# Optimization experiments

Hardware: AMD Instinct MI355X
Metric: run time of the kernel (lower is better)

## Reference

```python
import jax, jax.numpy as jnp
import numpy as np

B, S, HID = 2, 2048, 2048
H, HKV, DH = 32, 8, 64
GROUPS = H // HKV
SCALE = DH ** -0.5
ROPE_THETA = 10000.0
NEG_INF = jnp.finfo(jnp.float32).min


def setup_inputs() -> dict:
    key = jax.random.key(0)
    ks = jax.random.split(key, 6)
    hidden_states = jax.random.normal(ks[0], (B, S, HID), dtype=jnp.float32)
    # true rotary embeddings (HF Llama style): inv_freq over half dim, duplicated
    inv_freq = 1.0 / (ROPE_THETA ** (np.arange(0, DH, 2, dtype=np.float32) / DH))
    freqs = np.arange(S, dtype=np.float32)[:, None] * inv_freq[None, :]  # [S, DH/2]
    emb = np.concatenate([freqs, freqs], axis=-1)                        # [S, DH]
    cos = jnp.broadcast_to(jnp.asarray(np.cos(emb), jnp.float32), (B, S, DH))
    sin = jnp.broadcast_to(jnp.asarray(np.sin(emb), jnp.float32), (B, S, DH))
    # additive causal mask [1,1,S,S]
    causal = jnp.tril(jnp.ones((S, S), dtype=bool))
    attention_mask = jnp.where(causal, 0.0, NEG_INF)[None, None].astype(jnp.float32)
    std = 0.02
    Wq = jax.random.normal(ks[1], (H * DH, HID), dtype=jnp.float32) * std
    Wk = jax.random.normal(ks[2], (HKV * DH, HID), dtype=jnp.float32) * std
    Wv = jax.random.normal(ks[3], (HKV * DH, HID), dtype=jnp.float32) * std
    Wo = jax.random.normal(ks[4], (HID, H * DH), dtype=jnp.float32) * std
    return {"hidden_states": hidden_states, "cos": cos, "sin": sin,
            "attention_mask": attention_mask, "Wq": Wq, "Wk": Wk, "Wv": Wv, "Wo": Wo}


def _rotate_half(x):
    x1, x2 = jnp.split(x, 2, axis=-1)
    return jnp.concatenate([-x2, x1], axis=-1)


def reference(hidden_states, cos, sin, attention_mask, Wq, Wk, Wv, Wo):
    b, s, _ = hidden_states.shape
    # projections -> [B, H(kv), S, DH]
    q = (hidden_states @ Wq.T).reshape(b, s, H, DH).transpose(0, 2, 1, 3)
    k = (hidden_states @ Wk.T).reshape(b, s, HKV, DH).transpose(0, 2, 1, 3)
    v = (hidden_states @ Wv.T).reshape(b, s, HKV, DH).transpose(0, 2, 1, 3)
    # RoPE (cos/sin: [B,S,DH] -> broadcast over head axis)
    c = cos[:, None, :, :]
    sn = sin[:, None, :, :]
    q = q * c + _rotate_half(q) * sn
    k = k * c + _rotate_half(k) * sn
    # GQA: repeat kv heads
    k = jnp.repeat(k, GROUPS, axis=1)  # [B,H,S,DH]
    v = jnp.repeat(v, GROUPS, axis=1)
    # eager attention: full [B,H,S,S] scores in memory
    scores = jnp.einsum('bhqd,bhkd->bhqk', q, k) * SCALE + attention_mask[:, :, :, :s]
    attn = jax.nn.softmax(scores, axis=-1)
    out = jnp.einsum('bhqk,bhkd->bhqd', attn, v)
    out = out.transpose(0, 2, 1, 3).reshape(b, s, H * DH)
    return out @ Wo.T
```

## Files before the change

### kernel.cpp

```cpp
#include <hip/hip_runtime.h>
#include <hip/hip_bf16.h>
#include <cstdint>
#include <cstddef>

#define B_    2
#define S_    2048
#define HID_  2048
#define H_    32
#define HKV_  8
#define DH_   64
#define SC2_  0.1803368801111244f

typedef __bf16 bf16;
typedef bf16  bf16x2 __attribute__((ext_vector_type(2)));
typedef bf16  bf16x4 __attribute__((ext_vector_type(4)));
typedef bf16  bf16x8 __attribute__((ext_vector_type(8)));
typedef float f32x4  __attribute__((ext_vector_type(4)));
typedef float f32x16 __attribute__((ext_vector_type(16)));
typedef uint32_t u32x2 __attribute__((ext_vector_type(2)));

typedef __attribute__((address_space(3))) uint32_t  lds_u32_t;
typedef __attribute__((address_space(1))) const uint32_t glob_u32_t;

__device__ __forceinline__ void async16(const void* g, void* l) {
    __builtin_amdgcn_global_load_lds((glob_u32_t*)g, (lds_u32_t*)l, 16, 0, 0);
}

__device__ __forceinline__ bf16x8 cvt8(float4 a, float4 b) {
    bf16x8 r;
    r[0] = (bf16)a.x; r[1] = (bf16)a.y; r[2] = (bf16)a.z; r[3] = (bf16)a.w;
    r[4] = (bf16)b.x; r[5] = (bf16)b.y; r[6] = (bf16)b.z; r[7] = (bf16)b.w;
    return r;
}

__device__ __forceinline__ uint32_t pkbf(float a, float b) {
    bf16x2 t; t[0] = (bf16)a; t[1] = (bf16)b;
    return __builtin_bit_cast(uint32_t, t);
}
__device__ __forceinline__ bf16x8 mk8(uint32_t a, uint32_t b, uint32_t c, uint32_t d) {
    union { uint32_t u[4]; bf16x8 v; } t;
    t.u[0] = a; t.u[1] = b; t.u[2] = c; t.u[3] = d;
    return t.v;
}

#define WAIT_N_BARRIER(N_ASM)                              \
    asm volatile(N_ASM ::: "memory");                      \
    __builtin_amdgcn_s_barrier();                          \
    __builtin_amdgcn_sched_barrier(0);

#define END_BARRIER()                                      \
    __builtin_amdgcn_sched_barrier(0);                     \
    __builtin_amdgcn_s_barrier();

__global__ __launch_bounds__(256) void cvt_all_kernel(
    const float* __restrict__ X,  const float* __restrict__ Wq,
    const float* __restrict__ Wk, const float* __restrict__ Wv,
    const float* __restrict__ Wo,
    bf16* __restrict__ Xb,  bf16* __restrict__ Wqb, bf16* __restrict__ Wkb,
    bf16* __restrict__ Wvb, bf16* __restrict__ Wob)
{
    const int i = blockIdx.x * 256 + threadIdx.x;
    const float* src; bf16* dst; int off;
    if (i < 1048576)      { src = X;  dst = Xb;  off = i; }
    else if (i < 1572864) { src = Wq; dst = Wqb; off = i - 1048576; }
    else if (i < 1703936) { src = Wk; dst = Wkb; off = i - 1572864; }
    else if (i < 1835008) { src = Wv; dst = Wvb; off = i - 1703936; }
    else                  { src = Wo; dst = Wob; off = i - 1835008; }
    float4 a = ((const float4*)src)[2 * off];
    float4 b = ((const float4*)src)[2 * off + 1];
    ((bf16x8*)dst)[off] = cvt8(a, b);
}

__global__ __launch_bounds__(256) void gemm_qkv_kernel(
    const bf16* __restrict__ A,
    const bf16* __restrict__ Wqb, const bf16* __restrict__ Wkb,
    const bf16* __restrict__ Wvb,
    const float* __restrict__ cs, const float* __restrict__ sn,
    bf16* __restrict__ Qo, bf16* __restrict__ Ko, bf16* __restrict__ Vt)
{
    __shared__ bf16 a_lds[2][128 * 64];
    __shared__ bf16 b_lds[2][128 * 64];

    const int tid  = threadIdx.x;
    const int wave = tid >> 6;
    const int lane = tid & 63;
    const int quad = lane >> 4;
    const int l16  = lane & 15;
    const int wm   = wave >> 1;
    const int wn   = wave & 1;

    const int idx = blockIdx.x + 32 * blockIdx.y;
    const int swz = (idx & 7) * 96 + (idx >> 3);
    const int m0  = (swz & 31) * 128;
    const int n0  = (swz >> 5) * 128;

    f32x4 acc[4][4];
    #pragma unroll
    for (int mt = 0; mt < 4; ++mt)
        #pragma unroll
        for (int nt = 0; nt < 4; ++nt)
            acc[mt][nt] = (f32x4){0.f, 0.f, 0.f, 0.f};

    int srow[4], sgcol[4];
    const bf16* browp[4];
    #pragma unroll
    for (int i = 0; i < 4; ++i) {
        const int e = tid * 8 + i * 2048;
        srow[i] = e >> 6;
        const int chunk = (e >> 3) & 7;
        sgcol[i] = (chunk ^ (srow[i] & 7)) << 3;
        const int n = n0 + srow[i];
        browp[i] = (n < 2048) ? (Wqb + (size_t)n * HID_)
                 : (n < 2560) ? (Wkb + (size_t)(n - 2048) * HID_)
                              : (Wvb + (size_t)(n - 2560) * HID_);
    }

    #pragma unroll
    for (int i = 0; i < 4; ++i) {
        async16(A + (size_t)(m0 + srow[i]) * HID_ + sgcol[i],
                &a_lds[0][tid * 8 + i * 2048]);
        async16(browp[i] + sgcol[i],
                &b_lds[0][tid * 8 + i * 2048]);
    }

    for (int k0 = 0; k0 < HID_; k0 += 64) {
        const int cur = (k0 >> 6) & 1;
        if (k0 + 64 < HID_) {
            #pragma unroll
            for (int i = 0; i < 4; ++i) {
                async16(A + (size_t)(m0 + srow[i]) * HID_ + k0 + 64 + sgcol[i],
                        &a_lds[cur ^ 1][tid * 8 + i * 2048]);
                async16(browp[i] + k0 + 64 + sgcol[i],
                        &b_lds[cur ^ 1][tid * 8 + i * 2048]);
            }
            WAIT_N_BARRIER("s_waitcnt vmcnt(8)");
        } else {
            WAIT_N_BARRIER("s_waitcnt vmcnt(0)");
        }
        const bf16* al = a_lds[cur];
        const bf16* bl = b_lds[cur];
        #pragma unroll
        for (int ks = 0; ks < 2; ++ks) {
            bf16x8 af[4], bfr[4];
            #pragma unroll
            for (int mt = 0; mt < 4; ++mt) {
                const int row = wm * 64 + mt * 16 + l16;
                const int c = (ks * 4 + quad) ^ (row & 7);
                af[mt] = *(const bf16x8*)(&al[row * 64 + c * 8]);
            }
            #pragma unroll
            for (int nt = 0; nt < 4; ++nt) {
                const int row = wn * 64 + nt * 16 + l16;
                const int c = (ks * 4 + quad) ^ (row & 7);
                bfr[nt] = *(const bf16x8*)(&bl[row * 64 + c * 8]);
            }
            #pragma unroll
            for (int mt = 0; mt < 4; ++mt)
                #pragma unroll
                for (int nt = 0; nt < 4; ++nt)
                    acc[mt][nt] = __builtin_amdgcn_mfma_f32_16x16x32_bf16(
                        af[mt], bfr[nt], acc[mt][nt], 0, 0, 0);
        }
        END_BARRIER();
    }

    const int nw = n0 + wn * 64;
    const int d  = l16;
    #pragma unroll
    for (int mt = 0; mt < 4; ++mt) {
        #pragma unroll
        for (int r = 0; r < 4; ++r) {
            const int m  = m0 + wm * 64 + mt * 16 + quad * 4 + r;
            const int bb = m >> 11;
            const int ss = m & (S_ - 1);
            const float v0 = acc[mt][0][r], v1 = acc[mt][1][r];
            const float v2 = acc[mt][2][r], v3 = acc[mt][3][r];
            if (nw < 2048) {
                const int h = nw >> 6;
                bf16* dp = Qo + ((size_t)(bb * H_ + h) * S_ + ss) * DH_;
                const float* cp = cs + ((size_t)bb * S_ + ss) * DH_;
                const float* sp = sn + ((size_t)bb * S_ + ss) * DH_;
                dp[ 0 + d] = (bf16)((v0 * cp[ 0 + d] - v2 * sp[ 0 + d]) * SC2_);
                dp[16 + d] = (bf16)((v1 * cp[16 + d] - v3 * sp[16 + d]) * SC2_);
                dp[32 + d] = (bf16)((v2 * cp[32 + d] + v0 * sp[32 + d]) * SC2_);
                dp[48 + d] = (bf16)((v3 * cp[48 + d] + v1 * sp[48 + d]) * SC2_);
            } else if (nw < 2560) {
                const int h = (nw - 2048) >> 6;
                bf16* dp = Ko + ((size_t)(bb * HKV_ + h) * S_ + ss) * DH_;
                const float* cp = cs + ((size_t)bb * S_ + ss) * DH_;
                const float* sp = sn + ((size_t)bb * S_ + ss) * DH_;
                dp[ 0 + d] = (bf16)(v0 * cp[ 0 + d] - v2 * sp[ 0 + d]);
                dp[16 + d] = (bf16)(v1 * cp[16 + d] - v3 * sp[16 + d]);
                dp[32 + d] = (bf16)(v2 * cp[32 + d] + v0 * sp[32 + d]);
                dp[48 + d] = (bf16)(v3 * cp[48 + d] + v1 * sp[48 + d]);
            } else {
                const int h = (nw - 2560) >> 6;
                bf16* dp = Vt + ((size_t)(bb * HKV_ + h) * DH_) * S_ + ss;
                dp[(size_t)( 0 + d) * S_] = (bf16)v0;
                dp[(size_t)(16 + d) * S_] = (bf16)v1;
                dp[(size_t)(32 + d) * S_] = (bf16)v2;
                dp[(size_t)(48 + d) * S_] = (bf16)v3;
            }
        }
    }
}

__global__ __launch_bounds__(256) void gemm_out_kernel(
    const bf16* __restrict__ A, const bf16* __restrict__ Wb,
    float* __restrict__ Y)
{
    __shared__ bf16 a_lds[2][128 * 64];
    __shared__ bf16 b_lds[2][128 * 64];

    const int tid  = threadIdx.x;
    const int wave = tid >> 6;
    const int lane = tid & 63;
    const int quad = lane >> 4;
    const int l16  = lane & 15;
    const int wm   = wave >> 1;
    const int wn   = wave & 1;

    const int idx = blockIdx.x + 32 * blockIdx.y;
    const int swz = (idx & 7) * 64 + (idx >> 3);
    const int m0  = (swz & 31) * 128;
    const int n0  = (swz >> 5) * 128;

    f32x4 acc[4][4];
    #pragma unroll
    for (int mt = 0; mt < 4; ++mt)
        #pragma unroll
        for (int nt = 0; nt < 4; ++nt)
            acc[mt][nt] = (f32x4){0.f, 0.f, 0.f, 0.f};

    int srow[4], sgcol[4];
    #pragma unroll
    for (int i = 0; i < 4; ++i) {
        const int e = tid * 8 + i * 2048;
        srow[i] = e >> 6;
        const int chunk = (e >> 3) & 7;
        sgcol[i] = (chunk ^ (srow[i] & 7)) << 3;
    }

    #pragma unroll
    for (int i = 0; i < 4; ++i) {
        async16(A + (size_t)(m0 + srow[i]) * HID_ + sgcol[i],
                &a_lds[0][tid * 8 + i * 2048]);
        async16(Wb + (size_t)(n0 + srow[i]) * HID_ + sgcol[i],
                &b_lds[0][tid * 8 + i * 2048]);
    }

    for (int k0 = 0; k0 < HID_; k0 += 64) {
        const int cur = (k0 >> 6) & 1;
        if (k0 + 64 < HID_) {
            #pragma unroll
            for (int i = 0; i < 4; ++i) {
                async16(A + (size_t)(m0 + srow[i]) * HID_ + k0 + 64 + sgcol[i],
                        &a_lds[cur ^ 1][tid * 8 + i * 2048]);
                async16(Wb + (size_t)(n0 + srow[i]) * HID_ + k0 + 64 + sgcol[i],
                        &b_lds[cur ^ 1][tid * 8 + i * 2048]);
            }
            WAIT_N_BARRIER("s_waitcnt vmcnt(8)");
        } else {
            WAIT_N_BARRIER("s_waitcnt vmcnt(0)");
        }
        const bf16* al = a_lds[cur];
        const bf16* bl = b_lds[cur];
        #pragma unroll
        for (int ks = 0; ks < 2; ++ks) {
            bf16x8 af[4], bfr[4];
            #pragma unroll
            for (int mt = 0; mt < 4; ++mt) {
                const int row = wm * 64 + mt * 16 + l16;
                const int c = (ks * 4 + quad) ^ (row & 7);
                af[mt] = *(const bf16x8*)(&al[row * 64 + c * 8]);
            }
            #pragma unroll
            for (int nt = 0; nt < 4; ++nt) {
                const int row = wn * 64 + nt * 16 + l16;
                const int c = (ks * 4 + quad) ^ (row & 7);
                bfr[nt] = *(const bf16x8*)(&bl[row * 64 + c * 8]);
            }
            #pragma unroll
            for (int mt = 0; mt < 4; ++mt)
                #pragma unroll
                for (int nt = 0; nt < 4; ++nt)
                    acc[mt][nt] = __builtin_amdgcn_mfma_f32_16x16x32_bf16(
                        af[mt], bfr[nt], acc[mt][nt], 0, 0, 0);
        }
        END_BARRIER();
    }

    #pragma unroll
    for (int mt = 0; mt < 4; ++mt)
        #pragma unroll
        for (int nt = 0; nt < 4; ++nt)
            #pragma unroll
            for (int r = 0; r < 4; ++r) {
                const int m = m0 + wm * 64 + mt * 16 + quad * 4 + r;
                const int n = n0 + wn * 64 + nt * 16 + l16;
                Y[(size_t)m * HID_ + n] = acc[mt][nt][r];
            }
}

__global__ __launch_bounds__(256) void attn_kernel(
    const bf16* __restrict__ Q, const bf16* __restrict__ K,
    const bf16* __restrict__ Vt, bf16* __restrict__ O)
{
    __shared__ bf16 k_lds[2][64 * 64];
    __shared__ bf16 v_lds[2][64 * 64];

    const int tid  = threadIdx.x;
    const int wave = tid >> 6;
    const int lane = tid & 63;
    const int l32  = lane & 31;
    const int half = lane >> 5;
    const int h  = blockIdx.y;
    const int b  = blockIdx.z;
    const int hkv = h >> 2;

    const bf16* Qg = Q  + (size_t)(b * H_ + h) * S_ * DH_;
    const bf16* Kg = K  + (size_t)(b * HKV_ + hkv) * S_ * DH_;
    const bf16* Vg = Vt + ((size_t)(b * HKV_ + hkv) * DH_) * S_;

    const int srow0  = tid >> 3;
    const int scolsw = ((tid & 7) ^ ((tid >> 3) & 7)) << 3;

    #pragma unroll 1
    for (int ph = 0; ph < 2; ++ph) {
        const int qt  = ph == 0 ? (int)blockIdx.x : (15 - (int)blockIdx.x);
        const int q0  = qt * 128;
        const int qb0 = q0 + wave * 32;
        const int qa  = qb0 + l32;

        bf16x8 qf[4];
        #pragma unroll
        for (int c = 0; c < 4; ++c)
            qf[c] = *(const bf16x8*)(Qg + (size_t)qa * DH_ + c * 16 + half * 8);

        f32x16 o_acc[2];
        #pragma unroll
        for (int dt = 0; dt < 2; ++dt)
            #pragma unroll
            for (int e = 0; e < 16; ++e) o_acc[dt][e] = 0.f;
        float m_i = -1e30f, l_i = 0.f;

        const int nkt = 2 * qt + 2;

        #pragma unroll
        for (int i = 0; i < 2; ++i) {
            const int row = srow0 + i * 32;
            async16(Kg + (size_t)row * DH_ + scolsw, &k_lds[0][tid * 8 + i * 2048]);
            async16(Vg + (size_t)row * S_  + scolsw, &v_lds[0][tid * 8 + i * 2048]);
        }

        for (int kt = 0; kt < nkt; ++kt) {
            if (kt + 1 < nkt) {
                bf16* kb = k_lds[(kt + 1) & 1];
                bf16* vb = v_lds[(kt + 1) & 1];
                #pragma unroll
                for (int i = 0; i < 2; ++i) {
                    const int row = srow0 + i * 32;
                    async16(Kg + (size_t)((kt + 1) * 64 + row) * DH_ + scolsw,
                            kb + tid * 8 + i * 2048);
                    async16(Vg + (size_t)row * S_ + (kt + 1) * 64 + scolsw,
                            vb + tid * 8 + i * 2048);
                }
                WAIT_N_BARRIER("s_waitcnt vmcnt(4)");
            } else {
                WAIT_N_BARRIER("s_waitcnt vmcnt(0)");
            }

            if (kt * 64 <= qb0 + 31) {
                const bf16* kb = k_lds[kt & 1];
                const bf16* vb = v_lds[kt & 1];
                const bool act1 = (kt * 64 + 32) <= (qb0 + 31);

                f32x16 s0, s1;
                {
                    bf16x8 kf[4];
                    #pragma unroll
                    for (int c = 0; c < 4; ++c) {
                        const int col = ((2 * c + half) ^ (l32 & 7)) << 3;
                        kf[c] = *(const bf16x8*)(kb + l32 * 64 + col);
                    }
                    f32x16 a;
                    #pragma unroll
                    for (int e = 0; e < 16; ++e) a[e] = 0.f;
                    __builtin_amdgcn_s_setprio(1);
                    #pragma unroll
                    for (int c = 0; c < 4; ++c)
                        a = __builtin_amdgcn_mfma_f32_32x32x16_bf16(kf[c], qf[c], a, 0, 0, 0);
                    __builtin_amdgcn_s_setprio(0);
                    s0 = a;
                }
                if (act1) {
                    bf16x8 kf[4];
                    #pragma unroll
                    for (int c = 0; c < 4; ++c) {
                        const int row = 32 + l32;
                        const int col = ((2 * c + half) ^ (row & 7)) << 3;
                        kf[c] = *(const bf16x8*)(kb + row * 64 + col);
                    }
                    f32x16 a;
                    #pragma unroll
                    for (int e = 0; e < 16; ++e) a[e] = 0.f;
                    __builtin_amdgcn_s_setprio(1);
                    #pragma unroll
                    for (int c = 0; c < 4; ++c)
                        a = __builtin_amdgcn_mfma_f32_32x32x16_bf16(kf[c], qf[c], a, 0, 0, 0);
                    __builtin_amdgcn_s_setprio(0);
                    s1 = a;
                }

                if (!((kt * 64 + 31) <= qb0)) {
                    const int qrel = qa - kt * 64 - 4 * half;
                    #pragma unroll
                    for (int e = 0; e < 16; ++e)
                        if (((e & 3) + 8 * (e >> 2)) > qrel) s0[e] = -1e30f;
                }
                if (act1 && !((kt * 64 + 63) <= qb0)) {
                    const int qrel = qa - kt * 64 - 32 - 4 * half;
                    #pragma unroll
                    for (int e = 0; e < 16; ++e)
                        if (((e & 3) + 8 * (e >> 2)) > qrel) s1[e] = -1e30f;
                }

                float mx = s0[0];
                #pragma unroll
                for (int e = 1; e < 16; ++e) mx = fmaxf(mx, s0[e]);
                if (act1)
                    #pragma unroll
                    for (int e = 0; e < 16; ++e) mx = fmaxf(mx, s1[e]);
                mx = fmaxf(mx, __shfl_xor(mx, 32));

                float al = 1.f;
                if (!__all(mx <= m_i + 8.f)) {
                    const float mn = fmaxf(m_i, mx);
                    al = exp2f(m_i - mn);
                    m_i = mn;
                    #pragma unroll
                    for (int dt = 0; dt < 2; ++dt)
                        #pragma unroll
                        for (int e = 0; e < 16; ++e) o_acc[dt][e] *= al;
                }

                float sm = 0.f;
                #pragma unroll
                for (int e = 0; e < 16; ++e) {
                    const float pp = exp2f(s0[e] - m_i);
                    s0[e] = pp; sm += pp;
                }
                if (act1)
                    #pragma unroll
                    for (int e = 0; e < 16; ++e) {
                        const float pp = exp2f(s1[e] - m_i);
                        s1[e] = pp; sm += pp;
                    }
                sm += __shfl_xor(sm, 32);
                l_i = l_i * al + sm;

                bf16x8 pf[4];
                {
                    uint32_t d0 = pkbf(s0[0],  s0[1]),  d1 = pkbf(s0[2],  s0[3]);
                    uint32_t d2 = pkbf(s0[4],  s0[5]),  d3 = pkbf(s0[6],  s0[7]);
                    uint32_t d4 = pkbf(s0[8],  s0[9]),  d5 = pkbf(s0[10], s0[11]);
                    uint32_t d6 = pkbf(s0[12], s0[13]), d7 = pkbf(s0[14], s0[15]);
                    u32x2 r02 = __builtin_amdgcn_permlane32_swap(d0, d2, false, false);
                    u32x2 r13 = __builtin_amdgcn_permlane32_swap(d1, d3, false, false);
                    u32x2 r46 = __builtin_amdgcn_permlane32_swap(d4, d6, false, false);
                    u32x2 r57 = __builtin_amdgcn_permlane32_swap(d5, d7, false, false);
                    pf[0] = mk8(r02[0], r13[0], r02[1], r13[1]);
                    pf[1] = mk8(r46[0], r57[0], r46[1], r57[1]);
                }
                if (act1) {
                    uint32_t d0 = pkbf(s1[0],  s1[1]),  d1 = pkbf(s1[2],  s1[3]);
                    uint32_t d2 = pkbf(s1[4],  s1[5]),  d3 = pkbf(s1[6],  s1[7]);
                    uint32_t d4 = pkbf(s1[8],  s1[9]),  d5 = pkbf(s1[10], s1[11]);
                    uint32_t d6 = pkbf(s1[12], s1[13]), d7 = pkbf(s1[14], s1[15]);
                    u32x2 r02 = __builtin_amdgcn_permlane32_swap(d0, d2, false, false);
                    u32x2 r13 = __builtin_amdgcn_permlane32_swap(d1, d3, false, false);
                    u32x2 r46 = __builtin_amdgcn_permlane32_swap(d4, d6, false, false);
                    u32x2 r57 = __builtin_amdgcn_permlane32_swap(d5, d7, false, false);
                    pf[2] = mk8(r02[0], r13[0], r02[1], r13[1]);
                    pf[3] = mk8(r46[0], r57[0], r46[1], r57[1]);
                }

                bf16x8 vf[2][4];
                #pragma unroll
                for (int dt = 0; dt < 2; ++dt)
                    #pragma unroll
                    for (int c = 0; c < 4; ++c) {
                        const int row = dt * 32 + l32;
                        const int col = ((2 * c + half) ^ (row & 7)) << 3;
                        vf[dt][c] = *(const bf16x8*)(vb + row * 64 + col);
                    }

                const int nc = act1 ? 4 : 2;
                __builtin_amdgcn_s_setprio(1);
                #pragma unroll
                for (int c = 0; c < 4; ++c) {
                    if (c >= nc) break;
                    #pragma unroll
                    for (int dt = 0; dt < 2; ++dt)
                        o_acc[dt] = __builtin_amdgcn_mfma_f32_32x32x16_bf16(
                            vf[dt][c], pf[c], o_acc[dt], 0, 0, 0);
                }
                __builtin_amdgcn_s_setprio(0);
            }
            END_BARRIER();
        }

        const float inv = 1.f / l_i;
        bf16* op = O + ((size_t)(b * S_ + qa) * H_ + h) * DH_;
        #pragma unroll
        for (int dt = 0; dt < 2; ++dt)
            #pragma unroll
            for (int g = 0; g < 4; ++g) {
                bf16x4 ov;
                #pragma unroll
                for (int r = 0; r < 4; ++r) ov[r] = (bf16)(o_acc[dt][g * 4 + r] * inv);
                *(bf16x4*)(op + dt * 32 + g * 8 + half * 4) = ov;
            }
        __builtin_amdgcn_s_barrier();
    }
}

extern "C" void kernel_launch(void* const* d_in, const int* in_sizes, int n_in,
                              void* d_out, int out_size, void* d_ws, size_t ws_size,
                              hipStream_t stream)
{
    const float* X    = (const float*)d_in[0];
    const float* cs   = (const float*)d_in[1];
    const float* sn   = (const float*)d_in[2];
    const float* Wq   = (const float*)d_in[4];
    const float* Wk   = (const float*)d_in[5];
    const float* Wv   = (const float*)d_in[6];
    const float* Wo   = (const float*)d_in[7];
    float* Y          = (float*)d_out;

    bf16* Xb  = (bf16*)d_ws;
    bf16* Wqb = Xb  + (size_t)8388608;
    bf16* Wkb = Wqb + (size_t)4194304;
    bf16* Wvb = Wkb + (size_t)1048576;
    bf16* Wob = Wvb + (size_t)1048576;
    bf16* Qb  = Wob + (size_t)4194304;
    bf16* Kb  = Qb  + (size_t)8388608;
    bf16* Vtb = Kb  + (size_t)2097152;
    bf16* Ob  = Vtb + (size_t)2097152;

    dim3 blk(256);
    cvt_all_kernel<<<dim3(9216), blk, 0, stream>>>(X, Wq, Wk, Wv, Wo,
                                                   Xb, Wqb, Wkb, Wvb, Wob);
    gemm_qkv_kernel<<<dim3(32, 24), blk, 0, stream>>>(Xb, Wqb, Wkb, Wvb,
                                                      cs, sn, Qb, Kb, Vtb);
    attn_kernel<<<dim3(8, H_, B_), blk, 0, stream>>>(Qb, Kb, Vtb, Ob);
    gemm_out_kernel<<<dim3(32, 16), blk, 0, stream>>>(Ob, Wob, Y);
}
```

Measured before the change: 350.6 us.

## Use 512-thread attention blocks over 256-row query tiles with LPT-ordered 1D grid

The attention kernel now runs 8 waves per block, each handling 32 query rows of a 256-row tile, instead of 4 waves processing two balanced 128-row tiles in sequence. The grid becomes 512 one-dimensional blocks ordered so the heaviest causal tiles (largest qt) launch first for load balance. Each K/V tile loaded into LDS is now shared by twice as many waves, so one async load per thread fills a buffer. The trade-off is less even per-block work: imbalance now relies on scheduling order rather than pairing, and more waves wait at each barrier.

```diff
diff --git a/kernel.cpp b/kernel.cpp
--- a/kernel.cpp
+++ b/kernel.cpp
@@ -302,7 +302,7 @@
             }
 }
 
-__global__ __launch_bounds__(256) void attn_kernel(
+__global__ __launch_bounds__(512) void attn_kernel(
     const bf16* __restrict__ Q, const bf16* __restrict__ K,
     const bf16* __restrict__ Vt, bf16* __restrict__ O)
 {
@@ -314,215 +314,205 @@
     const int lane = tid & 63;
     const int l32  = lane & 31;
     const int half = lane >> 5;
-    const int h  = blockIdx.y;
-    const int b  = blockIdx.z;
+
+    const int j  = blockIdx.x;
+    const int bh = j & 63;
+    const int h  = bh & 31;
+    const int b  = bh >> 5;
+    const int a  = j >> 6;
+    const int qt = (a < 4) ? (7 - a) : (a - 4);
     const int hkv = h >> 2;
 
     const bf16* Qg = Q  + (size_t)(b * H_ + h) * S_ * DH_;
     const bf16* Kg = K  + (size_t)(b * HKV_ + hkv) * S_ * DH_;
     const bf16* Vg = Vt + ((size_t)(b * HKV_ + hkv) * DH_) * S_;
 
-    const int srow0  = tid >> 3;
-    const int scolsw = ((tid & 7) ^ ((tid >> 3) & 7)) << 3;
-
-    #pragma unroll 1
-    for (int ph = 0; ph < 2; ++ph) {
-        const int qt  = ph == 0 ? (int)blockIdx.x : (15 - (int)blockIdx.x);
-        const int q0  = qt * 128;
-        const int qb0 = q0 + wave * 32;
-        const int qa  = qb0 + l32;
-
-        bf16x8 qf[4];
-        #pragma unroll
-        for (int c = 0; c < 4; ++c)
-            qf[c] = *(const bf16x8*)(Qg + (size_t)qa * DH_ + c * 16 + half * 8);
-
-        f32x16 o_acc[2];
-        #pragma unroll
-        for (int dt = 0; dt < 2; ++dt)
-            #pragma unroll
-            for (int e = 0; e < 16; ++e) o_acc[dt][e] = 0.f;
-        float m_i = -1e30f, l_i = 0.f;
-
-        const int nkt = 2 * qt + 2;
-
-        #pragma unroll
-        for (int i = 0; i < 2; ++i) {
-            const int row = srow0 + i * 32;
-            async16(Kg + (size_t)row * DH_ + scolsw, &k_lds[0][tid * 8 + i * 2048]);
-            async16(Vg + (size_t)row * S_  + scolsw, &v_lds[0][tid * 8 + i * 2048]);
-        }
-
-        for (int kt = 0; kt < nkt; ++kt) {
-            if (kt + 1 < nkt) {
-                bf16* kb = k_lds[(kt + 1) & 1];
-                bf16* vb = v_lds[(kt + 1) & 1];
-                #pragma unroll
-                for (int i = 0; i < 2; ++i) {
-                    const int row = srow0 + i * 32;
-                    async16(Kg + (size_t)((kt + 1) * 64 + row) * DH_ + scolsw,
-                            kb + tid * 8 + i * 2048);
-                    async16(Vg + (size_t)row * S_ + (kt + 1) * 64 + scolsw,
-                            vb + tid * 8 + i * 2048);
+    const int srow   = tid >> 3;
+    const int scolsw = ((tid & 7) ^ (srow & 7)) << 3;
+
+    const int qb0 = qt * 256 + wave * 32;
+    const int qa  = qb0 + l32;
+    const int nkt = 4 * qt + 4;
+
+    bf16x8 qf[4];
+    #pragma unroll
+    for (int c = 0; c < 4; ++c)
+        qf[c] = *(const bf16x8*)(Qg + (size_t)qa * DH_ + c * 16 + half * 8);
+
+    f32x16 o_acc[2];
+    #pragma unroll
+    for (int dt = 0; dt < 2; ++dt)
+        #pragma unroll
+        for (int e = 0; e < 16; ++e) o_acc[dt][e] = 0.f;
+    float m_i = -1e30f, l_i = 0.f;
+
+    async16(Kg + (size_t)srow * DH_ + scolsw, &k_lds[0][tid * 8]);
+    async16(Vg + (size_t)srow * S_  + scolsw, &v_lds[0][tid * 8]);
+
+    for (int kt = 0; kt < nkt; ++kt) {
+        if (kt + 1 < nkt) {
+            bf16* kb = k_lds[(kt + 1) & 1];
+            bf16* vb = v_lds[(kt + 1) & 1];
+            async16(Kg + (size_t)((kt + 1) * 64 + srow) * DH_ + scolsw,
+                    kb + tid * 8);
+            async16(Vg + (size_t)srow * S_ + (kt + 1) * 64 + scolsw,
+                    vb + tid * 8);
+            WAIT_N_BARRIER("s_waitcnt vmcnt(2)");
+        } else {
+            WAIT_N_BARRIER("s_waitcnt vmcnt(0)");
+        }
+
+        if (kt * 64 <= qb0 + 31) {
+            const bf16* kb = k_lds[kt & 1];
+            const bf16* vb = v_lds[kt & 1];
+            const bool act1 = (kt * 64 + 32) <= (qb0 + 31);
+
+            f32x16 s0, s1;
+            {
+                bf16x8 kf[4];
+                #pragma unroll
+                for (int c = 0; c < 4; ++c) {
+                    const int col = ((2 * c + half) ^ (l32 & 7)) << 3;
+                    kf[c] = *(const bf16x8*)(kb + l32 * 64 + col);
                 }
-                WAIT_N_BARRIER("s_waitcnt vmcnt(4)");
-            } else {
-                WAIT_N_BARRIER("s_waitcnt vmcnt(0)");
-            }
-
-            if (kt * 64 <= qb0 + 31) {
-                const bf16* kb = k_lds[kt & 1];
-                const bf16* vb = v_lds[kt & 1];
-                const bool act1 = (kt * 64 + 32) <= (qb0 + 31);
-
-                f32x16 s0, s1;
-                {
-                    bf16x8 kf[4];
-                    #pragma unroll
-                    for (int c = 0; c < 4; ++c) {
-                        const int col = ((2 * c + half) ^ (l32 & 7)) << 3;
-                        kf[c] = *(const bf16x8*)(kb + l32 * 64 + col);
-                    }
-                    f32x16 a;
-                    #pragma unroll
-                    for (int e = 0; e < 16; ++e) a[e] = 0.f;
-                    __builtin_amdgcn_s_setprio(1);
-                    #pragma unroll
-                    for (int c = 0; c < 4; ++c)
-                        a = __builtin_amdgcn_mfma_f32_32x32x16_bf16(kf[c], qf[c], a, 0, 0, 0);
-                    __builtin_amdgcn_s_setprio(0);
-                    s0 = a;
+                f32x16 acc;
+                #pragma unroll
+                for (int e = 0; e < 16; ++e) acc[e] = 0.f;
+                __builtin_amdgcn_s_setprio(1);
+                #pragma unroll
+                for (int c = 0; c < 4; ++c)
+                    acc = __builtin_amdgcn_mfma_f32_32x32x16_bf16(kf[c], qf[c], acc, 0, 0, 0);
+                __builtin_amdgcn_s_setprio(0);
+                s0 = acc;
+            }
+            if (act1) {
+                bf16x8 kf[4];
+                #pragma unroll
+                for (int c = 0; c < 4; ++c) {
+                    const int row = 32 + l32;
+                    const int col = ((2 * c + half) ^ (row & 7)) << 3;
+                    kf[c] = *(const bf16x8*)(kb + row * 64 + col);
                 }
-                if (act1) {
-                    bf16x8 kf[4];
-                    #pragma unroll
-                    for (int c = 0; c < 4; ++c) {
-                        const int row = 32 + l32;
-                        const int col = ((2 * c + half) ^ (row & 7)) << 3;
-                        kf[c] = *(const bf16x8*)(kb + row * 64 + col);
-                    }
-                    f32x16 a;
-                    #pragma unroll
-                    for (int e = 0; e < 16; ++e) a[e] = 0.f;
-                    __builtin_amdgcn_s_setprio(1);
-                    #pragma unroll
-                    for (int c = 0; c < 4; ++c)
-                        a = __builtin_amdgcn_mfma_f32_32x32x16_bf16(kf[c], qf[c], a, 0, 0, 0);
-                    __builtin_amdgcn_s_setprio(0);
-                    s1 = a;
-                }
-
-                if (!((kt * 64 + 31) <= qb0)) {
-                    const int qrel = qa - kt * 64 - 4 * half;
-                    #pragma unroll
-                    for (int e = 0; e < 16; ++e)
-                        if (((e & 3) + 8 * (e >> 2)) > qrel) s0[e] = -1e30f;
-                }
-                if (act1 && !((kt * 64 + 63) <= qb0)) {
-                    const int qrel = qa - kt * 64 - 32 - 4 * half;
-                    #pragma unroll
-                    for (int e = 0; e < 16; ++e)
-                        if (((e & 3) + 8 * (e >> 2)) > qrel) s1[e] = -1e30f;
-                }
-
-                float mx = s0[0];
-                #pragma unroll
-                for (int e = 1; e < 16; ++e) mx = fmaxf(mx, s0[e]);
-                if (act1)
-                    #pragma unroll
-                    for (int e = 0; e < 16; ++e) mx = fmaxf(mx, s1[e]);
-                mx = fmaxf(mx, __shfl_xor(mx, 32));
-
-                float al = 1.f;
-                if (!__all(mx <= m_i + 8.f)) {
-                    const float mn = fmaxf(m_i, mx);
-                    al = exp2f(m_i - mn);
-                    m_i = mn;
-                    #pragma unroll
-                    for (int dt = 0; dt < 2; ++dt)
-                        #pragma unroll
-                        for (int e = 0; e < 16; ++e) o_acc[dt][e] *= al;
-                }
-
-                float sm = 0.f;
-                #pragma unroll
-                for (int e = 0; e < 16; ++e) {
-                    const float pp = exp2f(s0[e] - m_i);
-                    s0[e] = pp; sm += pp;
-                }
-                if (act1)
-                    #pragma unroll
-                    for (int e = 0; e < 16; ++e) {
-                        const float pp = exp2f(s1[e] - m_i);
-                        s1[e] = pp; sm += pp;
-                    }
-                sm += __shfl_xor(sm, 32);
-                l_i = l_i * al + sm;
-
-                bf16x8 pf[4];
-                {
-                    uint32_t d0 = pkbf(s0[0],  s0[1]),  d1 = pkbf(s0[2],  s0[3]);
-                    uint32_t d2 = pkbf(s0[4],  s0[5]),  d3 = pkbf(s0[6],  s0[7]);
-                    uint32_t d4 = pkbf(s0[8],  s0[9]),  d5 = pkbf(s0[10], s0[11]);
-                    uint32_t d6 = pkbf(s0[12], s0[13]), d7 = pkbf(s0[14], s0[15]);
-                    u32x2 r02 = __builtin_amdgcn_permlane32_swap(d0, d2, false, false);
-                    u32x2 r13 = __builtin_amdgcn_permlane32_swap(d1, d3, false, false);
-                    u32x2 r46 = __builtin_amdgcn_permlane32_swap(d4, d6, false, false);
-                    u32x2 r57 = __builtin_amdgcn_permlane32_swap(d5, d7, false, false);
-                    pf[0] = mk8(r02[0], r13[0], r02[1], r13[1]);
-                    pf[1] = mk8(r46[0], r57[0], r46[1], r57[1]);
-                }
-                if (act1) {
-                    uint32_t d0 = pkbf(s1[0],  s1[1]),  d1 = pkbf(s1[2],  s1[3]);
-                    uint32_t d2 = pkbf(s1[4],  s1[5]),  d3 = pkbf(s1[6],  s1[7]);
-                    uint32_t d4 = pkbf(s1[8],  s1[9]),  d5 = pkbf(s1[10], s1[11]);
-                    uint32_t d6 = pkbf(s1[12], s1[13]), d7 = pkbf(s1[14], s1[15]);
-                    u32x2 r02 = __builtin_amdgcn_permlane32_swap(d0, d2, false, false);
-                    u32x2 r13 = __builtin_amdgcn_permlane32_swap(d1, d3, false, false);
-                    u32x2 r46 = __builtin_amdgcn_permlane32_swap(d4, d6, false, false);
-                    u32x2 r57 = __builtin_amdgcn_permlane32_swap(d5, d7, false, false);
-                    pf[2] = mk8(r02[0], r13[0], r02[1], r13[1]);
-                    pf[3] = mk8(r46[0], r57[0], r46[1], r57[1]);
-                }
-
-                bf16x8 vf[2][4];
+                f32x16 acc;
+                #pragma unroll
+                for (int e = 0; e < 16; ++e) acc[e] = 0.f;
+                __builtin_amdgcn_s_setprio(1);
+                #pragma unroll
+                for (int c = 0; c < 4; ++c)
+                    acc = __builtin_amdgcn_mfma_f32_32x32x16_bf16(kf[c], qf[c], acc, 0, 0, 0);
+                __builtin_amdgcn_s_setprio(0);
+                s1 = acc;
+            }
+
+            if (!((kt * 64 + 31) <= qb0)) {
+                const int qrel = qa - kt * 64 - 4 * half;
+                #pragma unroll
+                for (int e = 0; e < 16; ++e)
+                    if (((e & 3) + 8 * (e >> 2)) > qrel) s0[e] = -1e30f;
+            }
+            if (act1 && !((kt * 64 + 63) <= qb0)) {
+                const int qrel = qa - kt * 64 - 32 - 4 * half;
+                #pragma unroll
+                for (int e = 0; e < 16; ++e)
+                    if (((e & 3) + 8 * (e >> 2)) > qrel) s1[e] = -1e30f;
+            }
+
+            float mx = s0[0];
+            #pragma unroll
+            for (int e = 1; e < 16; ++e) mx = fmaxf(mx, s0[e]);
+            if (act1)
+                #pragma unroll
+                for (int e = 0; e < 16; ++e) mx = fmaxf(mx, s1[e]);
+            mx = fmaxf(mx, __shfl_xor(mx, 32));
+
+            float al = 1.f;
+            if (!__all(mx <= m_i + 8.f)) {
+                const float mn = fmaxf(m_i, mx);
+                al = exp2f(m_i - mn);
+                m_i = mn;
                 #pragma unroll
                 for (int dt = 0; dt < 2; ++dt)
                     #pragma unroll
-                    for (int c = 0; c < 4; ++c) {
-                        const int row = dt * 32 + l32;
-                        const int col = ((2 * c + half) ^ (row & 7)) << 3;
-                        vf[dt][c] = *(const bf16x8*)(vb + row * 64 + col);
-                    }
-
-                const int nc = act1 ? 4 : 2;
-                __builtin_amdgcn_s_setprio(1);
+                    for (int e = 0; e < 16; ++e) o_acc[dt][e] *= al;
+            }
+
+            float sm = 0.f;
+            #pragma unroll
+            for (int e = 0; e < 16; ++e) {
+                const float pp = exp2f(s0[e] - m_i);
+                s0[e] = pp; sm += pp;
+            }
+            if (act1)
+                #pragma unroll
+                for (int e = 0; e < 16; ++e) {
+                    const float pp = exp2f(s1[e] - m_i);
+                    s1[e] = pp; sm += pp;
+                }
+            sm += __shfl_xor(sm, 32);
+            l_i = l_i * al + sm;
+
+            bf16x8 pf[4];
+            {
+                uint32_t d0 = pkbf(s0[0],  s0[1]),  d1 = pkbf(s0[2],  s0[3]);
+                uint32_t d2 = pkbf(s0[4],  s0[5]),  d3 = pkbf(s0[6],  s0[7]);
+                uint32_t d4 = pkbf(s0[8],  s0[9]),  d5 = pkbf(s0[10], s0[11]);
+                uint32_t d6 = pkbf(s0[12], s0[13]), d7 = pkbf(s0[14], s0[15]);
+                u32x2 r02 = __builtin_amdgcn_permlane32_swap(d0, d2, false, false);
+                u32x2 r13 = __builtin_amdgcn_permlane32_swap(d1, d3, false, false);
+                u32x2 r46 = __builtin_amdgcn_permlane32_swap(d4, d6, false, false);
+                u32x2 r57 = __builtin_amdgcn_permlane32_swap(d5, d7, false, false);
+                pf[0] = mk8(r02[0], r13[0], r02[1], r13[1]);
+                pf[1] = mk8(r46[0], r57[0], r46[1], r57[1]);
+            }
+            if (act1) {
+                uint32_t d0 = pkbf(s1[0],  s1[1]),  d1 = pkbf(s1[2],  s1[3]);
+                uint32_t d2 = pkbf(s1[4],  s1[5]),  d3 = pkbf(s1[6],  s1[7]);
+                uint32_t d4 = pkbf(s1[8],  s1[9]),  d5 = pkbf(s1[10], s1[11]);
+                uint32_t d6 = pkbf(s1[12], s1[13]), d7 = pkbf(s1[14], s1[15]);
+                u32x2 r02 = __builtin_amdgcn_permlane32_swap(d0, d2, false, false);
+                u32x2 r13 = __builtin_amdgcn_permlane32_swap(d1, d3, false, false);
+                u32x2 r46 = __builtin_amdgcn_permlane32_swap(d4, d6, false, false);
+                u32x2 r57 = __builtin_amdgcn_permlane32_swap(d5, d7, false, false);
+                pf[2] = mk8(r02[0], r13[0], r02[1], r13[1]);
+                pf[3] = mk8(r46[0], r57[0], r46[1], r57[1]);
+            }
+
+            bf16x8 vf[2][4];
+            #pragma unroll
+            for (int dt = 0; dt < 2; ++dt)
                 #pragma unroll
                 for (int c = 0; c < 4; ++c) {
-                    if (c >= nc) break;
-                    #pragma unroll
-                    for (int dt = 0; dt < 2; ++dt)
-                        o_acc[dt] = __builtin_amdgcn_mfma_f32_32x32x16_bf16(
-                            vf[dt][c], pf[c], o_acc[dt], 0, 0, 0);
+                    const int row = dt * 32 + l32;
+                    const int col = ((2 * c + half) ^ (row & 7)) << 3;
+                    vf[dt][c] = *(const bf16x8*)(vb + row * 64 + col);
                 }
-                __builtin_amdgcn_s_setprio(0);
-            }
-            END_BARRIER();
-        }
-
-        const float inv = 1.f / l_i;
-        bf16* op = O + ((size_t)(b * S_ + qa) * H_ + h) * DH_;
-        #pragma unroll
-        for (int dt = 0; dt < 2; ++dt)
-            #pragma unroll
-            for (int g = 0; g < 4; ++g) {
-                bf16x4 ov;
-                #pragma unroll
-                for (int r = 0; r < 4; ++r) ov[r] = (bf16)(o_acc[dt][g * 4 + r] * inv);
-                *(bf16x4*)(op + dt * 32 + g * 8 + half * 4) = ov;
-            }
-        __builtin_amdgcn_s_barrier();
-    }
+
+            const int nc = act1 ? 4 : 2;
+            __builtin_amdgcn_s_setprio(1);
+            #pragma unroll
+            for (int c = 0; c < 4; ++c) {
+                if (c >= nc) break;
+                #pragma unroll
+                for (int dt = 0; dt < 2; ++dt)
+                    o_acc[dt] = __builtin_amdgcn_mfma_f32_32x32x16_bf16(
+                        vf[dt][c], pf[c], o_acc[dt], 0, 0, 0);
+            }
+            __builtin_amdgcn_s_setprio(0);
+        }
+        END_BARRIER();
+    }
+
+    const float inv = 1.f / l_i;
+    bf16* op = O + ((size_t)(b * S_ + qa) * H_ + h) * DH_;
+    #pragma unroll
+    for (int dt = 0; dt < 2; ++dt)
+        #pragma unroll
+        for (int g2 = 0; g2 < 4; ++g2) {
+            bf16x4 ov;
+            #pragma unroll
+            for (int r = 0; r < 4; ++r) ov[r] = (bf16)(o_acc[dt][g2 * 4 + r] * inv);
+            *(bf16x4*)(op + dt * 32 + g2 * 8 + half * 4) = ov;
+        }
 }
 
 extern "C" void kernel_launch(void* const* d_in, const int* in_sizes, int n_in,
@@ -553,6 +543,6 @@
                                                    Xb, Wqb, Wkb, Wvb, Wob);
     gemm_qkv_kernel<<<dim3(32, 24), blk, 0, stream>>>(Xb, Wqb, Wkb, Wvb,
                                                       cs, sn, Qb, Kb, Vtb);
-    attn_kernel<<<dim3(8, H_, B_), blk, 0, stream>>>(Qb, Kb, Vtb, Ob);
+    attn_kernel<<<dim3(512), dim3(512), 0, stream>>>(Qb, Kb, Vtb, Ob);
     gemm_out_kernel<<<dim3(32, 16), blk, 0, stream>>>(Ob, Wob, Y);
 }
```

Result: no change. 355.9 us (+1.5%).
